# Performance work log

Hardware: AMD Instinct MI355X
Metric: run time of the kernel (lower is better)

The kernel has to match this reference:

```python
import jax, jax.numpy as jnp
import numpy as np

N_NODES = 100000
D = 256
E = 1000000
H = 128


def setup_inputs() -> dict:
    key = jax.random.key(0)
    k1, k2, k3, k4 = jax.random.split(key, 4)
    z = jax.random.normal(k1, (N_NODES, D), dtype=jnp.float32)
    edge_label_index = jax.random.randint(k2, (2, E), 0, N_NODES, dtype=jnp.int64)
    # Linear layers: PyTorch Linear(in, out) -> weight [out, in]; stored here as [in, out].
    W1 = jax.random.normal(k3, (2 * D, H), dtype=jnp.float32) * (1.0 / np.sqrt(2 * D))
    b1 = jnp.zeros((H,), dtype=jnp.float32)
    W2 = jax.random.normal(k4, (H, 1), dtype=jnp.float32) * (1.0 / np.sqrt(H))
    b2 = jnp.zeros((1,), dtype=jnp.float32)
    return {"z": z, "edge_label_index": edge_label_index,
            "W1": W1, "b1": b1, "W2": W2, "b2": b2}


def reference(z, edge_label_index, W1, b1, W2, b2):
    src = edge_label_index[0]
    dst = edge_label_index[1]
    # Gather node pairs and concat: [E, 2*D]
    pair = jnp.concatenate([z[src], z[dst]], axis=-1)
    h = jax.nn.relu(pair @ W1 + b1)          # [E, H]
    out = (h @ W2 + b2).reshape(-1)          # [E]
    return out
```

## Files before the change

### kernel.cpp

```cpp
#include <hip/hip_runtime.h>
#include <hip/hip_bf16.h>


typedef __attribute__((ext_vector_type(4))) float floatx4;
typedef __attribute__((ext_vector_type(8))) short short8;
typedef _Float16 half8v __attribute__((ext_vector_type(8)));
typedef __fp16 fp16x2 __attribute__((ext_vector_type(2)));

#if defined(__has_builtin)
#if __has_builtin(__builtin_amdgcn_fdot2)
#define HAVE_FDOT2 1
#endif
#endif

__device__ __forceinline__ unsigned short bf16rne(float x) {
    unsigned int u = __float_as_uint(x);
    u += 0x7fffu + ((u >> 16) & 1u);
    return (unsigned short)(u >> 16);
}

__device__ __forceinline__ void gl_lds16(const void* g, void* l) {
    __builtin_amdgcn_global_load_lds(
        (const __attribute__((address_space(1))) void*)(unsigned long long)g,
        (__attribute__((address_space(3))) void*)(unsigned)(unsigned long long)l,
        16, 0, 0);
}

__global__ void cvt_w1h(const float* __restrict__ W1, unsigned short* __restrict__ BTc2) {
    int t = blockIdx.x * blockDim.x + threadIdx.x;
    int hf = t >> 15, rem = t & 32767;
    int s = rem >> 12, rem2 = rem & 4095;
    int n = rem2 >> 5, rem3 = rem2 & 31;
    int gp = rem3 >> 3, j = rem3 & 7;
    int g = gp ^ ((n >> 1) & 3);
    int k = hf * 256 + s * 32 + g * 8 + j;
    BTc2[t] = bf16rne(W1[k * 128 + n]);
}

__global__ void cvt_w1(const float* __restrict__ W1, unsigned short* __restrict__ BTc) {
    int t = blockIdx.x * blockDim.x + threadIdx.x;
    int s = t >> 12, rem = t & 4095;
    int n = rem >> 5, rem2 = rem & 31;
    int gp = rem2 >> 3, j = rem2 & 7;
    int g = gp ^ ((n >> 1) & 3);
    int k = s * 32 + g * 8 + j;
    BTc[t] = bf16rne(W1[k * 128 + n]);
}

__global__ __launch_bounds__(256, 2)
void gemm_hb(const float* __restrict__ zf, int nnodes,
             const unsigned short* __restrict__ BTc2,
             const float* __restrict__ b1, _Float16* __restrict__ Hh)
{
    const int t = threadIdx.x;
    const int wid = t >> 6;
    const int lane = t & 63;
    const int l15 = lane & 15;
    const int quad = lane >> 4;
    const int m0 = blockIdx.x * 128 + wid * 32;

    unsigned offs[2];
#pragma unroll
    for (int mf = 0; mf < 2; ++mf) {
        int r = m0 + mf * 16 + l15;
        r = r < nnodes ? r : nnodes - 1;
        offs[mf] = (unsigned)r * 1024u;
    }
    const char* zbb = (const char*)zf;

    const int swz = (l15 >> 1) & 3;
    const unsigned short* gb = BTc2 + l15 * 32 + (quad ^ swz) * 8;

    auto load_a = [&](int ks, short8* dst) {
        const int cb = ks * 128 + quad * 32;
#pragma unroll
        for (int mf = 0; mf < 2; ++mf) {
            const float* pf = (const float*)(zbb + (size_t)offs[mf] + cb);
            float4 f0 = *(const float4*)pf;
            float4 f1 = *(const float4*)(pf + 4);
            short8 av;
            av[0] = (short)bf16rne(f0.x); av[1] = (short)bf16rne(f0.y);
            av[2] = (short)bf16rne(f0.z); av[3] = (short)bf16rne(f0.w);
            av[4] = (short)bf16rne(f1.x); av[5] = (short)bf16rne(f1.y);
            av[6] = (short)bf16rne(f1.z); av[7] = (short)bf16rne(f1.w);
            dst[mf] = av;
        }
    };

    floatx4 acc[2][16];
#pragma unroll
    for (int mf = 0; mf < 2; ++mf)
#pragma unroll
        for (int nf = 0; nf < 16; ++nf)
            acc[mf][nf] = (floatx4){0.f, 0.f, 0.f, 0.f};

    short8 A[4][2];
    load_a(0, A[0]);
    load_a(1, A[1]);
    load_a(2, A[2]);

#pragma unroll
    for (int ks = 0; ks < 8; ++ks) {
        if (ks + 3 < 8) load_a(ks + 3, A[(ks + 3) & 3]);

        const short8* ac = A[ks & 3];

#pragma unroll
        for (int gq = 0; gq < 4; ++gq) {
            const unsigned short* bs =
                gb + (gq >> 1) * 32768 + ks * 4096 + (gq & 1) * 2048;
            short8 bfr[4];
#pragma unroll
            for (int nf = 0; nf < 4; ++nf)
                bfr[nf] = *(const short8*)(bs + nf * 512);
#pragma unroll
            for (int nf = 0; nf < 4; ++nf)
#pragma unroll
                for (int mf = 0; mf < 2; ++mf)
                    acc[mf][gq * 4 + nf] = __builtin_amdgcn_mfma_f32_16x16x32_bf16(
                        ac[mf], bfr[nf], acc[mf][gq * 4 + nf], 0, 0, 0);
        }
    }

    float b1v[8];
#pragma unroll
    for (int nf = 0; nf < 8; ++nf)
        b1v[nf] = b1[nf * 16 + l15];
#pragma unroll
    for (int mf = 0; mf < 2; ++mf) {
#pragma unroll
        for (int r = 0; r < 4; ++r) {
            int row = m0 + mf * 16 + quad * 4 + r;
            if (row < nnodes) {
                _Float16* hp = Hh + (size_t)row * 256 + l15;
#pragma unroll
                for (int nf = 0; nf < 8; ++nf)
                    hp[nf * 16] = (_Float16)(acc[mf][nf][r] + b1v[nf]);
#pragma unroll
                for (int nf = 0; nf < 8; ++nf)
                    hp[128 + nf * 16] = (_Float16)acc[mf][8 + nf][r];
            }
        }
    }
}

__global__ __launch_bounds__(256)
void edge_out(const _Float16* __restrict__ Hh, const int* __restrict__ eli,
              int E, int nnodes,
              const float* __restrict__ W2, const float* __restrict__ b2,
              float* __restrict__ out)
{
    const int t = threadIdx.x;
    const int lane = t & 63;
    const int wid = t >> 6;
    const int l15 = lane & 15;
    const int grp = lane >> 4;

    fp16x2 w2h[4];
#pragma unroll
    for (int p = 0; p < 4; ++p) {
        w2h[p][0] = (__fp16)W2[l15 * 8 + 2 * p];
        w2h[p][1] = (__fp16)W2[l15 * 8 + 2 * p + 1];
    }
    const float b2s = b2[0];

    const int e0 = blockIdx.x * 64 + wid * 16 + grp;

    half8v hs[4], hd[4];
    int ee[4];
#pragma unroll
    for (int i = 0; i < 4; ++i) {
        int e = e0 + i * 4;
        ee[i] = e;
        int ec = e < E ? e : E - 1;
        int s = eli[ec];
        int d = eli[E + ec];
        s = s < 0 ? 0 : (s >= nnodes ? nnodes - 1 : s);
        d = d < 0 ? 0 : (d >= nnodes ? nnodes - 1 : d);
        hs[i] = *(const half8v*)(Hh + (size_t)s * 256 + l15 * 8);
        hd[i] = *(const half8v*)(Hh + (size_t)d * 256 + 128 + l15 * 8);
    }
    const half8v zero = {};
#pragma unroll
    for (int i = 0; i < 4; ++i) {
        half8v v = hs[i] + hd[i];
        v = __builtin_elementwise_max(v, zero);
        float sacc = 0.f;
#if defined(HAVE_FDOT2)
#pragma unroll
        for (int p = 0; p < 4; ++p) {
            fp16x2 a;
            a[0] = (__fp16)v[2 * p];
            a[1] = (__fp16)v[2 * p + 1];
            sacc = __builtin_amdgcn_fdot2(a, w2h[p], sacc, false);
        }
#else
#pragma unroll
        for (int p = 0; p < 4; ++p) {
            sacc = fmaf((float)v[2 * p],     (float)w2h[p][0], sacc);
            sacc = fmaf((float)v[2 * p + 1], (float)w2h[p][1], sacc);
        }
#endif
        sacc += __shfl_xor(sacc, 1);
        sacc += __shfl_xor(sacc, 2);
        sacc += __shfl_xor(sacc, 4);
        sacc += __shfl_xor(sacc, 8);
        if (l15 == 0 && ee[i] < E)
            out[ee[i]] = sacc + b2s;
    }
}

__global__ __launch_bounds__(256, 2)
void fused_mlp_f32(const float* __restrict__ zf, const int* __restrict__ eli,
                   int E, int nnodes,
                   const unsigned short* __restrict__ BTc,
                   const float* __restrict__ b1, const float* __restrict__ W2,
                   const float* __restrict__ b2, float* __restrict__ out)
{
    __shared__ unsigned short btile[2][4][128][32];

    const int t = threadIdx.x;
    const int wid = t >> 6;
    const int lane = t & 63;
    const int l15 = lane & 15;
    const int quad = lane >> 4;
    const int m0 = blockIdx.x * 256 + wid * 64;

    unsigned offs[4], offd[4];
#pragma unroll
    for (int mf = 0; mf < 4; ++mf) {
        int e = m0 + mf * 16 + l15;
        e = e < E ? e : E - 1;
        int s = eli[e];
        int d = eli[E + e];
        s = s < 0 ? 0 : (s >= nnodes ? nnodes - 1 : s);
        d = d < 0 ? 0 : (d >= nnodes ? nnodes - 1 : d);
        offs[mf] = (unsigned)s * 1024u;
        offd[mf] = (unsigned)d * 1024u;
    }
    const char* zbb = (const char*)zf;

    const int swz = (l15 >> 1) & 3;
    const unsigned short* bbase = &btile[0][0][0][0] + l15 * 32 + (quad ^ swz) * 8;

    auto stage = [&](int kc, int buf) {
        const char* g = (const char*)BTc + kc * 32768 + wid * 1024 + lane * 16;
        char* l = (char*)&btile[buf][0][0][0] + wid * 1024 + lane * 16;
#pragma unroll
        for (int i = 0; i < 8; ++i)
            gl_lds16(g + i * 4096, l + i * 4096);
    };

    auto load_a = [&](int ks, short8* dst) {
        const unsigned* off = (ks < 8) ? offs : offd;
        const int cb = (ks & 7) * 128 + quad * 32;
#pragma unroll
        for (int mf = 0; mf < 4; ++mf) {
            const float* pf = (const float*)(zbb + (size_t)off[mf] + cb);
            float4 f0 = *(const float4*)pf;
            float4 f1 = *(const float4*)(pf + 4);
            short8 av;
            av[0] = (short)bf16rne(f0.x); av[1] = (short)bf16rne(f0.y);
            av[2] = (short)bf16rne(f0.z); av[3] = (short)bf16rne(f0.w);
            av[4] = (short)bf16rne(f1.x); av[5] = (short)bf16rne(f1.y);
            av[6] = (short)bf16rne(f1.z); av[7] = (short)bf16rne(f1.w);
            dst[mf] = av;
        }
    };

    floatx4 acc[4][8];
#pragma unroll
    for (int mf = 0; mf < 4; ++mf)
#pragma unroll
        for (int nf = 0; nf < 8; ++nf)
            acc[mf][nf] = (floatx4){0.f, 0.f, 0.f, 0.f};

    short8 A[3][4];
    stage(0, 0);
    load_a(0, A[0]);
    load_a(1, A[1]);
    __syncthreads();

#pragma unroll
    for (int kc = 0; kc < 4; ++kc) {
        if (kc < 3) stage(kc + 1, (kc + 1) & 1);

#pragma unroll
        for (int s4 = 0; s4 < 4; ++s4) {
            const int ks = kc * 4 + s4;
            if (ks + 2 < 16) load_a(ks + 2, A[(ks + 2) % 3]);

            const unsigned short* bs = bbase + (kc & 1) * 16384 + s4 * 4096;
            short8 bfr[8];
#pragma unroll
            for (int nf = 0; nf < 8; ++nf)
                bfr[nf] = *(const short8*)(bs + nf * 512);

            const short8* ac = A[ks % 3];
#pragma unroll
            for (int nf = 0; nf < 8; ++nf)
#pragma unroll
                for (int mf = 0; mf < 4; ++mf)
                    acc[mf][nf] = __builtin_amdgcn_mfma_f32_16x16x32_bf16(
                        ac[mf], bfr[nf], acc[mf][nf], 0, 0, 0);
        }

        if (kc < 3) __syncthreads();
    }

    const float b2s = b2[0];
    float b1v[8], w2v[8];
#pragma unroll
    for (int nf = 0; nf < 8; ++nf) {
        int c = nf * 16 + l15;
        b1v[nf] = b1[c];
        w2v[nf] = W2[c];
    }
#pragma unroll
    for (int mf = 0; mf < 4; ++mf) {
#pragma unroll
        for (int r = 0; r < 4; ++r) {
            float s = 0.f;
#pragma unroll
            for (int nf = 0; nf < 8; ++nf) {
                float v = acc[mf][nf][r] + b1v[nf];
                v = v > 0.f ? v : 0.f;
                s = fmaf(v, w2v[nf], s);
            }
            s += __shfl_xor(s, 1);
            s += __shfl_xor(s, 2);
            s += __shfl_xor(s, 4);
            s += __shfl_xor(s, 8);
            if (l15 == 0) {
                int e = m0 + mf * 16 + quad * 4 + r;
                if (e < E) out[e] = s + b2s;
            }
        }
    }
}

__global__ void naive_edge(const float* __restrict__ z, const int* __restrict__ eli,
                           int E, int nnodes,
                           const float* __restrict__ W1, const float* __restrict__ b1,
                           const float* __restrict__ W2, const float* __restrict__ b2,
                           float* __restrict__ out)
{
    __shared__ float red[2];
    int e = blockIdx.x;
    int j = threadIdx.x;
    int s = eli[e], d = eli[E + e];
    s = s < 0 ? 0 : (s >= nnodes ? nnodes - 1 : s);
    d = d < 0 ? 0 : (d >= nnodes ? nnodes - 1 : d);
    const float* zs = z + (long long)s * 256;
    const float* zd = z + (long long)d * 256;
    float h = b1[j];
    for (int i = 0; i < 256; ++i) h = fmaf(zs[i], W1[i * 128 + j], h);
    for (int i = 0; i < 256; ++i) h = fmaf(zd[i], W1[(256 + i) * 128 + j], h);
    h = h > 0.f ? h : 0.f;
    float v = h * W2[j];
    v += __shfl_xor(v, 1);  v += __shfl_xor(v, 2);  v += __shfl_xor(v, 4);
    v += __shfl_xor(v, 8);  v += __shfl_xor(v, 16); v += __shfl_xor(v, 32);
    if ((threadIdx.x & 63) == 0) red[threadIdx.x >> 6] = v;
    __syncthreads();
    if (threadIdx.x == 0) out[e] = red[0] + red[1] + b2[0];
}

extern "C" void kernel_launch(void* const* d_in, const int* in_sizes, int n_in,
                              void* d_out, int out_size, void* d_ws, size_t ws_size,
                              hipStream_t stream) {
    const float* z   = (const float*)d_in[0];
    const int*   eli = (const int*)d_in[1];
    const float* W1  = (const float*)d_in[2];
    const float* b1  = (const float*)d_in[3];
    const float* W2  = (const float*)d_in[4];
    const float* b2  = (const float*)d_in[5];
    float*       out = (float*)d_out;

    const int E      = in_sizes[1] / 2;
    const int nnodes = in_sizes[0] / 256;

    const size_t HB   = (size_t)nnodes * 512;
    const size_t BT2B = 131072;
    const size_t BTB  = (size_t)512 * 128 * 2;

    const int grid_gemm = (nnodes + 127) / 128;
    const int grid_edge = (E + 63) / 64;

    if (ws_size >= HB + BT2B) {
        _Float16*       Hh   = (_Float16*)d_ws;
        unsigned short* BTc2 = (unsigned short*)((char*)d_ws + HB);
        cvt_w1h<<<256, 256, 0, stream>>>(W1, BTc2);
        gemm_hb<<<grid_gemm, 256, 0, stream>>>(z, nnodes, BTc2, b1, Hh);
        edge_out<<<grid_edge, 256, 0, stream>>>(Hh, eli, E, nnodes, W2, b2, out);
    } else if (ws_size >= BTB) {
        unsigned short* BTc = (unsigned short*)d_ws;
        cvt_w1<<<256, 256, 0, stream>>>(W1, BTc);
        fused_mlp_f32<<<(E + 255) / 256, 256, 0, stream>>>(z, eli, E, nnodes, BTc, b1, W2, b2, out);
    } else {
        naive_edge<<<E, 128, 0, stream>>>(z, eli, E, nnodes, W1, b1, W2, b2, out);
    }
}
```

Before: 284.4 us.

## Make node GEMM persistent with W1 half staged in LDS per block

The per-node projection GEMM becomes a persistent kernel of 512 blocks. Each block loads one half of the bf16 W1 (64 KB) into shared memory once and loops over row tiles, computing only 128 output columns with half the accumulators. Previously every block streamed B fragments from global/L2 for all 256 columns. The change cuts B traffic and register pressure, but each z row is now read twice (once per half) and the 64 KB LDS footprint limits occupancy.

New measurement: 316.2 us. +11.2%, slower.

```diff
diff --git a/kernel.cpp b/kernel.cpp
--- a/kernel.cpp
+++ b/kernel.cpp
@@ -48,67 +48,86 @@
 }
 
 __global__ __launch_bounds__(256, 2)
-void gemm_hb(const float* __restrict__ zf, int nnodes,
+void gemm_hp(const float* __restrict__ zf, int nnodes,
              const unsigned short* __restrict__ BTc2,
              const float* __restrict__ b1, _Float16* __restrict__ Hh)
 {
+    __shared__ unsigned short B[32768];
+
     const int t = threadIdx.x;
     const int wid = t >> 6;
     const int lane = t & 63;
     const int l15 = lane & 15;
     const int quad = lane >> 4;
-    const int m0 = blockIdx.x * 128 + wid * 32;
-
-    unsigned offs[2];
-#pragma unroll
-    for (int mf = 0; mf < 2; ++mf) {
-        int r = m0 + mf * 16 + l15;
-        r = r < nnodes ? r : nnodes - 1;
-        offs[mf] = (unsigned)r * 1024u;
-    }
+    const int hf = blockIdx.x & 1;
+    const int b2 = blockIdx.x >> 1;
+    const int ntiles = (nnodes + 127) >> 7;
+
+    {
+        const char* g = (const char*)(BTc2 + hf * 32768) + t * 16;
+        char* l = (char*)B + t * 16;
+#pragma unroll
+        for (int i = 0; i < 16; ++i)
+            gl_lds16(g + i * 4096, l + i * 4096);
+    }
+    __syncthreads();
+
+    const int swz = (l15 >> 1) & 3;
+    const unsigned short* bbase = B + l15 * 32 + (quad ^ swz) * 8;
+
+    float b1v[8];
+#pragma unroll
+    for (int nf = 0; nf < 8; ++nf)
+        b1v[nf] = (hf == 0) ? b1[nf * 16 + l15] : 0.f;
+
     const char* zbb = (const char*)zf;
 
-    const int swz = (l15 >> 1) & 3;
-    const unsigned short* gb = BTc2 + l15 * 32 + (quad ^ swz) * 8;
-
-    auto load_a = [&](int ks, short8* dst) {
-        const int cb = ks * 128 + quad * 32;
+    for (int tile = b2; tile < ntiles; tile += 256) {
+        const int m0 = tile * 128 + wid * 32;
+
+        unsigned offs[2];
 #pragma unroll
         for (int mf = 0; mf < 2; ++mf) {
-            const float* pf = (const float*)(zbb + (size_t)offs[mf] + cb);
-            float4 f0 = *(const float4*)pf;
-            float4 f1 = *(const float4*)(pf + 4);
-            short8 av;
-            av[0] = (short)bf16rne(f0.x); av[1] = (short)bf16rne(f0.y);
-            av[2] = (short)bf16rne(f0.z); av[3] = (short)bf16rne(f0.w);
-            av[4] = (short)bf16rne(f1.x); av[5] = (short)bf16rne(f1.y);
-            av[6] = (short)bf16rne(f1.z); av[7] = (short)bf16rne(f1.w);
-            dst[mf] = av;
-        }
-    };
-
-    floatx4 acc[2][16];
-#pragma unroll
-    for (int mf = 0; mf < 2; ++mf)
-#pragma unroll
-        for (int nf = 0; nf < 16; ++nf)
-            acc[mf][nf] = (floatx4){0.f, 0.f, 0.f, 0.f};
-
-    short8 A[4][2];
-    load_a(0, A[0]);
-    load_a(1, A[1]);
-    load_a(2, A[2]);
-
-#pragma unroll
-    for (int ks = 0; ks < 8; ++ks) {
-        if (ks + 3 < 8) load_a(ks + 3, A[(ks + 3) & 3]);
-
-        const short8* ac = A[ks & 3];
-
-#pragma unroll
-        for (int gq = 0; gq < 4; ++gq) {
-            const unsigned short* bs =
-                gb + (gq >> 1) * 32768 + ks * 4096 + (gq & 1) * 2048;
+            int r = m0 + mf * 16 + l15;
+            r = r < nnodes ? r : nnodes - 1;
+            offs[mf] = (unsigned)r * 1024u;
+        }
+
+        auto load_a = [&](int ks, short8* dst) {
+            const int cb = ks * 128 + quad * 32;
+#pragma unroll
+            for (int mf = 0; mf < 2; ++mf) {
+                const float* pf = (const float*)(zbb + (size_t)offs[mf] + cb);
+                float4 f0 = *(const float4*)pf;
+                float4 f1 = *(const float4*)(pf + 4);
+                short8 av;
+                av[0] = (short)bf16rne(f0.x); av[1] = (short)bf16rne(f0.y);
+                av[2] = (short)bf16rne(f0.z); av[3] = (short)bf16rne(f0.w);
+                av[4] = (short)bf16rne(f1.x); av[5] = (short)bf16rne(f1.y);
+                av[6] = (short)bf16rne(f1.z); av[7] = (short)bf16rne(f1.w);
+                dst[mf] = av;
+            }
+        };
+
+        floatx4 acc[2][8];
+#pragma unroll
+        for (int mf = 0; mf < 2; ++mf)
+#pragma unroll
+            for (int nf = 0; nf < 8; ++nf)
+                acc[mf][nf] = (floatx4){0.f, 0.f, 0.f, 0.f};
+
+        short8 A[4][2];
+        load_a(0, A[0]);
+        load_a(1, A[1]);
+        load_a(2, A[2]);
+
+#pragma unroll
+        for (int ks = 0; ks < 8; ++ks) {
+            if (ks + 3 < 8) load_a(ks + 3, A[(ks + 3) & 3]);
+
+            const unsigned short* bs = bbase + ks * 4096;
+            const short8* ac = A[ks & 3];
+
             short8 bfr[4];
 #pragma unroll
             for (int nf = 0; nf < 4; ++nf)
@@ -117,28 +136,30 @@
             for (int nf = 0; nf < 4; ++nf)
 #pragma unroll
                 for (int mf = 0; mf < 2; ++mf)
-                    acc[mf][gq * 4 + nf] = __builtin_amdgcn_mfma_f32_16x16x32_bf16(
-                        ac[mf], bfr[nf], acc[mf][gq * 4 + nf], 0, 0, 0);
-        }
-    }
-
-    float b1v[8];
-#pragma unroll
-    for (int nf = 0; nf < 8; ++nf)
-        b1v[nf] = b1[nf * 16 + l15];
-#pragma unroll
-    for (int mf = 0; mf < 2; ++mf) {
-#pragma unroll
-        for (int r = 0; r < 4; ++r) {
-            int row = m0 + mf * 16 + quad * 4 + r;
-            if (row < nnodes) {
-                _Float16* hp = Hh + (size_t)row * 256 + l15;
-#pragma unroll
-                for (int nf = 0; nf < 8; ++nf)
-                    hp[nf * 16] = (_Float16)(acc[mf][nf][r] + b1v[nf]);
-#pragma unroll
-                for (int nf = 0; nf < 8; ++nf)
-                    hp[128 + nf * 16] = (_Float16)acc[mf][8 + nf][r];
+                    acc[mf][nf] = __builtin_amdgcn_mfma_f32_16x16x32_bf16(
+                        ac[mf], bfr[nf], acc[mf][nf], 0, 0, 0);
+#pragma unroll
+            for (int nf = 0; nf < 4; ++nf)
+                bfr[nf] = *(const short8*)(bs + (nf + 4) * 512);
+#pragma unroll
+            for (int nf = 0; nf < 4; ++nf)
+#pragma unroll
+                for (int mf = 0; mf < 2; ++mf)
+                    acc[mf][nf + 4] = __builtin_amdgcn_mfma_f32_16x16x32_bf16(
+                        ac[mf], bfr[nf], acc[mf][nf + 4], 0, 0, 0);
+        }
+
+#pragma unroll
+        for (int mf = 0; mf < 2; ++mf) {
+#pragma unroll
+            for (int r = 0; r < 4; ++r) {
+                int row = m0 + mf * 16 + quad * 4 + r;
+                if (row < nnodes) {
+                    _Float16* hp = Hh + (size_t)row * 256 + hf * 128 + l15;
+#pragma unroll
+                    for (int nf = 0; nf < 8; ++nf)
+                        hp[nf * 16] = (_Float16)(acc[mf][nf][r] + b1v[nf]);
+                }
             }
         }
     }
@@ -383,14 +404,13 @@
     const size_t BT2B = 131072;
     const size_t BTB  = (size_t)512 * 128 * 2;
 
-    const int grid_gemm = (nnodes + 127) / 128;
     const int grid_edge = (E + 63) / 64;
 
     if (ws_size >= HB + BT2B) {
         _Float16*       Hh   = (_Float16*)d_ws;
         unsigned short* BTc2 = (unsigned short*)((char*)d_ws + HB);
         cvt_w1h<<<256, 256, 0, stream>>>(W1, BTc2);
-        gemm_hb<<<grid_gemm, 256, 0, stream>>>(z, nnodes, BTc2, b1, Hh);
+        gemm_hp<<<512, 256, 0, stream>>>(z, nnodes, BTc2, b1, Hh);
         edge_out<<<grid_edge, 256, 0, stream>>>(Hh, eli, E, nnodes, W2, b2, out);
     } else if (ws_size >= BTB) {
         unsigned short* BTc = (unsigned short*)d_ws;
```
